# Performance work log

Hardware: AMD Instinct MI355X
Metric: run time of the kernel (lower is better)

## Reference

```python
import jax, jax.numpy as jnp
import numpy as np

B, S, E, NH = 2, 1024, 2048, 16
DH = E // NH
EPS = 1e-6

def setup_inputs() -> dict:
    key = jax.random.key(0)
    ks = jax.random.split(key, 6)
    q = jax.random.normal(ks[0], (B, S, E), dtype=jnp.float32)
    k = jax.random.normal(ks[1], (B, S, E), dtype=jnp.float32)
    v = jax.random.normal(ks[2], (B, S, E), dtype=jnp.float32)
    Wi = jax.random.normal(ks[3], (3 * E, NH), dtype=jnp.float32) * 0.02
    bi = jax.random.normal(ks[4], (NH,), dtype=jnp.float32) * 0.1
    Wf = jax.random.normal(ks[5], (3 * E, NH), dtype=jnp.float32) * 0.02
    bf = jnp.linspace(3.0, 6.0, NH, dtype=jnp.float32)  # bias_linspace_initializer(3,6)
    ln_scale = jnp.ones((E,), dtype=jnp.float32)
    return {"q": q, "k": k, "v": v, "Wi": Wi, "bi": bi, "Wf": Wf, "bf": bf, "ln_scale": ln_scale}

def _mlstm_forward(q, k, v, Wi, bi, Wf, bf, ln_scale):
    b, s, e = q.shape
    nh = Wi.shape[1]
    dh = e // nh
    x = jnp.concatenate([q, k, v], axis=-1)                     # (B,S,3E)
    ig = (x @ Wi + bi).transpose(0, 2, 1)[..., None]            # (B,NH,S,1)
    fg = (x @ Wf + bf).transpose(0, 2, 1)[..., None]            # (B,NH,S,1)
    split = lambda t: t.reshape(b, s, nh, dh).transpose(0, 2, 1, 3)
    qh, kh, vh = split(q), split(k), split(v)                   # (B,NH,S,DH)
    # parallel_stabilized_simple backend
    log_f = jax.nn.log_sigmoid(fg)                              # (B,NH,S,1)
    log_f_cum = jnp.concatenate(
        [jnp.zeros((b, nh, 1, 1), q.dtype), jnp.cumsum(log_f, axis=2)], axis=2
    )                                                           # (B,NH,S+1,1)
    # D[i,j] = cumsum[i] - cumsum[j] on causal part
    fg_mat = log_f_cum - jnp.transpose(log_f_cum, (0, 1, 3, 2)) # (B,NH,S+1,S+1)
    ltr = jnp.tril(jnp.ones((s, s), dtype=bool))
    log_fg = jnp.where(ltr, fg_mat[:, :, 1:, 1:], -jnp.inf)     # (B,NH,S,S)
    log_D = log_fg + jnp.transpose(ig, (0, 1, 3, 2))            # + i_j per column
    max_log_D = jnp.max(log_D, axis=-1, keepdims=True)          # (B,NH,S,1)
    D = jnp.exp(log_D - max_log_D)
    qk = jnp.einsum('bhsd,bhtd->bhst', qh, kh) / jnp.sqrt(jnp.asarray(dh, q.dtype))
    C = qk * D                                                  # (B,NH,S,S)
    normalizer = jnp.maximum(jnp.abs(C.sum(-1, keepdims=True)), jnp.exp(-max_log_D))
    Cn = C / (normalizer + EPS)
    h = jnp.einsum('bhst,bhtd->bhsd', Cn, vh)                   # (B,NH,S,DH)
    # MultiHeadLayerNorm: normalize over DH per head, scale (no bias)
    mu = h.mean(-1, keepdims=True)
    var = ((h - mu) ** 2).mean(-1, keepdims=True)
    hn = (h - mu) * jax.lax.rsqrt(var + EPS)
    hn = hn * ln_scale.reshape(1, nh, 1, dh)
    return hn.transpose(0, 2, 1, 3).reshape(b, s, e)            # (B,S,E)

def reference(q, k, v, Wi, bi, Wf, bf, ln_scale):
    return _mlstm_forward(q, k, v, Wi, bi, Wf, bf, ln_scale)
```

## Files before the change

### kernel.cpp

```cpp
#include <hip/hip_runtime.h>
#include <hip/hip_bf16.h>

#define B_   2
#define S_   1024
#define E_   2048
#define NH_  16
#define DH_  128
#define EPS_ 1e-6f

using half8   = __attribute__((ext_vector_type(8))) _Float16;
using floatx4 = __attribute__((ext_vector_type(4))) float;

__device__ __forceinline__ half8 cvt8h(const float* __restrict__ p) {
    float4 a = *(const float4*)p;
    float4 b = *(const float4*)(p + 4);
    half8 r;
    r[0] = (_Float16)a.x; r[1] = (_Float16)a.y;
    r[2] = (_Float16)a.z; r[3] = (_Float16)a.w;
    r[4] = (_Float16)b.x; r[5] = (_Float16)b.y;
    r[6] = (_Float16)b.z; r[7] = (_Float16)b.w;
    return r;
}

__global__ __launch_bounds__(256, 4) void gates_kernel(
    const float* __restrict__ q, const float* __restrict__ k,
    const float* __restrict__ v, const float* __restrict__ Wi,
    const float* __restrict__ Wf, float* __restrict__ pre_i,
    float* __restrict__ pre_f, _Float16* __restrict__ qhg,
    _Float16* __restrict__ khg, _Float16* __restrict__ vtg)
{
    __shared__ __attribute__((aligned(16))) _Float16 xs[32 * 264];
    __shared__ __attribute__((aligned(16))) _Float16 wt[32 * 264];

    const int t    = threadIdx.x;
    const int w    = t >> 6, lane = t & 63, quad = lane >> 4, l15 = lane & 15;
    const int mw   = w & 1, nw = w >> 1;
    const int m0   = blockIdx.x * 32;
    const int by   = blockIdx.y;
    const int kbase = by * 768;
    const int bblk = m0 >> 10;
    const int s0   = m0 & 1023;

    floatx4 acc = {0.f, 0.f, 0.f, 0.f};

    for (int c = 0; c < 3; ++c) {
        __syncthreads();
        const int e0   = kbase + c * 256;
        const int tsel = e0 >> 11;
        const int el0  = e0 & 2047;
        const float* xb = (tsel == 0) ? q : (tsel == 1) ? k : v;
        _Float16* fout = (tsel == 0) ? qhg : khg;
        #pragma unroll
        for (int i = 0; i < 4; ++i) {
            int g = t + i * 256;
            int row = g >> 5, grp = g & 31;
            half8 s8 = cvt8h(xb + (size_t)(m0 + row) * E_ + el0 + grp * 8);
            *(half8*)(&xs[row * 264 + grp * 8]) = s8;
            if (tsel < 2) {
                int el = el0 + grp * 8;
                int h  = el >> 7, d = el & 127;
                *(half8*)(fout + ((size_t)(bblk * NH_ + h) * S_ + s0 + row) * DH_ + d) = s8;
            }
        }
        {
            const int kk = t;
            const float* wiRow = Wi + (size_t)(e0 + kk) * NH_;
            const float* wfRow = Wf + (size_t)(e0 + kk) * NH_;
            float wif[16], wff[16];
            #pragma unroll
            for (int i4 = 0; i4 < 4; ++i4) {
                float4 a = *(const float4*)(wiRow + i4 * 4);
                wif[i4*4+0]=a.x; wif[i4*4+1]=a.y; wif[i4*4+2]=a.z; wif[i4*4+3]=a.w;
                float4 b = *(const float4*)(wfRow + i4 * 4);
                wff[i4*4+0]=b.x; wff[i4*4+1]=b.y; wff[i4*4+2]=b.z; wff[i4*4+3]=b.w;
            }
            #pragma unroll
            for (int hh = 0; hh < 16; ++hh) wt[hh * 264 + kk]        = (_Float16)wif[hh];
            #pragma unroll
            for (int hh = 0; hh < 16; ++hh) wt[(16 + hh) * 264 + kk] = (_Float16)wff[hh];
        }
        __syncthreads();
        if (tsel == 2) {
            const int col = t;
            const int el  = el0 + col;
            const int h   = el >> 7, d = el & 127;
            _Float16 tmp[32];
            #pragma unroll
            for (int r = 0; r < 32; ++r) tmp[r] = xs[r * 264 + col];
            const size_t vo = ((size_t)(bblk * NH_ + h) * DH_ + d) * S_ + s0;
            #pragma unroll
            for (int i = 0; i < 4; ++i)
                *(half8*)(vtg + vo + i * 8) = *(half8*)(&tmp[i * 8]);
        }
        #pragma unroll
        for (int ks = 0; ks < 8; ++ks) {
            half8 af = *(const half8*)(&xs[(mw * 16 + l15) * 264 + ks * 32 + quad * 8]);
            half8 bw = *(const half8*)(&wt[(nw * 16 + l15) * 264 + ks * 32 + quad * 8]);
            acc = __builtin_amdgcn_mfma_f32_16x16x32_f16(af, bw, acc, 0, 0, 0);
        }
    }
    #pragma unroll
    for (int reg = 0; reg < 4; ++reg) {
        int m   = m0 + mw * 16 + quad * 4 + reg;
        int b   = m >> 10, s = m & 1023;
        int col = nw * 16 + l15;
        float vacc = acc[reg];
        if (col < 16)
            pre_i[((size_t)(by * 32 + b * NH_ + col)) * S_ + s] = vacc;
        else
            pre_f[((size_t)(by * 32 + b * NH_ + col - 16)) * S_ + s] = vacc;
    }
}

__global__ __launch_bounds__(1024, 1) void scan_kernel(
    const float* __restrict__ pre_i, const float* __restrict__ pre_f,
    float* __restrict__ Aj, float* __restrict__ Cq,
    float* __restrict__ NFo, const float* __restrict__ bi,
    const float* __restrict__ bfb)
{
    __shared__ float wsumF[16], wmaxA[16];
    const int bh   = blockIdx.x;
    const int h    = bh & 15;
    const int t    = threadIdx.x;
    const int lane = t & 63, wv = t >> 6;

    float igv = bi[h], x = bfb[h];
    #pragma unroll
    for (int y = 0; y < 8; ++y) {
        igv += pre_i[((size_t)(y * 32 + bh)) * S_ + t];
        x   += pre_f[((size_t)(y * 32 + bh)) * S_ + t];
    }
    float lfv = (x >= 0.f) ? -log1pf(__expf(-x)) : (x - log1pf(__expf(x)));

    float sc = lfv;
    #pragma unroll
    for (int off = 1; off < 64; off <<= 1) {
        float o = __shfl_up(sc, off);
        if (lane >= off) sc += o;
    }
    if (lane == 63) wsumF[wv] = sc;
    __syncthreads();
    float Foff = 0.f;
    for (int i = 0; i < wv; ++i) Foff += wsumF[i];
    float F = Foff + sc;
    float a = igv - F;

    float ms = a;
    #pragma unroll
    for (int off = 1; off < 64; off <<= 1) {
        float o = __shfl_up(ms, off);
        if (lane >= off) ms = fmaxf(ms, o);
    }
    if (lane == 63) wmaxA[wv] = ms;
    __syncthreads();
    float Moff = -3.0e38f;
    for (int i = 0; i < wv; ++i) Moff = fmaxf(Moff, wmaxA[i]);
    float M = fmaxf(Moff, ms);

    size_t o = (size_t)bh * S_ + t;
    Aj[o]  = a;
    Cq[o]  = -M;
    NFo[o] = expf(fminf(-(F + M), 80.f));
}

__global__ __launch_bounds__(256, 1) void attn_kernel(
    const _Float16* __restrict__ qh, const _Float16* __restrict__ kh,
    const _Float16* __restrict__ vtg, const float* __restrict__ Aj,
    const float* __restrict__ Cq, const float* __restrict__ NFi,
    const float* __restrict__ lnsc, float* __restrict__ out)
{
    __shared__ __attribute__((aligned(16))) _Float16 Ks[64 * 136];
    __shared__ __attribute__((aligned(16))) _Float16 Vt[128 * 72];
    __shared__ __attribute__((aligned(16))) _Float16 Pb[128 * 72];
    __shared__ float aj[64];

    const int t    = threadIdx.x;
    const int w    = t >> 6, lane = t & 63, quad = lane >> 4, l15 = lane & 15;
    const int bid  = blockIdx.x;
    const int bh   = bid & 31;
    const int qpi  = bid >> 5;
    const int b    = bh >> 4, h = bh & 15;
    const int myq  = (w < 2) ? qpi : (15 - qpi);
    const int ktN  = 15 - qpi;
    const int qrow0 = myq * 64 + (w & 1) * 32;
    const int prow0 = w * 32;
    const int krow = t >> 2, kd0 = (t & 3) * 32;
    const int vd   = t >> 1, vj0 = (t & 1) * 32;

    float ci_r[2][4], nfv_r[2][4];
    #pragma unroll
    for (int s = 0; s < 2; ++s)
        #pragma unroll
        for (int reg = 0; reg < 4; ++reg) {
            int rl = qrow0 + s * 16 + quad * 4 + reg;
            ci_r[s][reg]  = Cq[(size_t)bh * S_ + rl];
            nfv_r[s][reg] = NFi[(size_t)bh * S_ + rl];
        }
    half8 aq[2][4];
    #pragma unroll
    for (int s = 0; s < 2; ++s) {
        const _Float16* qrow = qh + ((size_t)bh * S_ + qrow0 + s * 16 + l15) * DH_;
        #pragma unroll
        for (int ks = 0; ks < 4; ++ks)
            aq[s][ks] = *(const half8*)(qrow + ks * 32 + quad * 8);
    }

    half8 kreg[4], vreg[4];
    float ajreg = 0.f;
    {
        const _Float16* kp = kh + ((size_t)bh * S_ + krow) * DH_ + kd0;
        const _Float16* vp = vtg + ((size_t)bh * DH_ + vd) * S_ + vj0;
        #pragma unroll
        for (int i = 0; i < 4; ++i) { kreg[i] = *(const half8*)(kp + i * 8);
                                      vreg[i] = *(const half8*)(vp + i * 8); }
    }
    if (t < 64) ajreg = Aj[(size_t)bh * S_ + t];

    #pragma unroll
    for (int i = 0; i < 4; ++i) {
        *(half8*)(&Ks[krow * 136 + kd0 + i * 8]) = kreg[i];
        *(half8*)(&Vt[vd * 72 + vj0 + i * 8])    = vreg[i];
    }
    if (t < 64) aj[t] = ajreg;
    __syncthreads();

    floatx4 acc_h[2][8];
    #pragma unroll
    for (int s = 0; s < 2; ++s)
        #pragma unroll
        for (int i = 0; i < 8; ++i) acc_h[s][i] = (floatx4){0.f, 0.f, 0.f, 0.f};
    float lrun[2][4] = {{0.f, 0.f, 0.f, 0.f}, {0.f, 0.f, 0.f, 0.f}};
    const float rscale = 0.08838834764831845f;

    for (int kt = 0; kt <= ktN; ++kt) {
        if (kt < ktN) {
            const int j0n = (kt + 1) * 64;
            const _Float16* kp = kh + ((size_t)bh * S_ + j0n + krow) * DH_ + kd0;
            const _Float16* vp = vtg + ((size_t)bh * DH_ + vd) * S_ + j0n + vj0;
            #pragma unroll
            for (int i = 0; i < 4; ++i) { kreg[i] = *(const half8*)(kp + i * 8);
                                          vreg[i] = *(const half8*)(vp + i * 8); }
            if (t < 64) ajreg = Aj[(size_t)bh * S_ + j0n + t];
        }

        if (kt <= myq) {
            floatx4 sacc[2][4];
            #pragma unroll
            for (int s = 0; s < 2; ++s)
                #pragma unroll
                for (int nt = 0; nt < 4; ++nt) sacc[s][nt] = (floatx4){0.f, 0.f, 0.f, 0.f};
            #pragma unroll
            for (int ks = 0; ks < 4; ++ks) {
                #pragma unroll
                for (int nt = 0; nt < 4; ++nt) {
                    half8 bk = *(const half8*)(&Ks[(nt * 16 + l15) * 136 + ks * 32 + quad * 8]);
                    sacc[0][nt] = __builtin_amdgcn_mfma_f32_16x16x32_f16(aq[0][ks], bk, sacc[0][nt], 0, 0, 0);
                    sacc[1][nt] = __builtin_amdgcn_mfma_f32_16x16x32_f16(aq[1][ks], bk, sacc[1][nt], 0, 0, 0);
                }
            }
            const bool diag = (kt == myq);
            #pragma unroll
            for (int nt = 0; nt < 4; ++nt) {
                int jl = nt * 16 + l15;
                float a_j = aj[jl];
                #pragma unroll
                for (int s = 0; s < 2; ++s) {
                    #pragma unroll
                    for (int reg = 0; reg < 4; ++reg) {
                        int rloc = (w & 1) * 32 + s * 16 + quad * 4 + reg;
                        float p = 0.f;
                        if (!diag || (jl <= rloc))
                            p = sacc[s][nt][reg] * rscale * __expf(fminf(ci_r[s][reg] + a_j, 0.f));
                        lrun[s][reg] += p;
                        Pb[(prow0 + s * 16 + quad * 4 + reg) * 72 + jl] = (_Float16)p;
                    }
                }
            }
            #pragma unroll
            for (int ks2 = 0; ks2 < 2; ++ks2) {
                half8 ap0 = *(const half8*)(&Pb[(prow0 + l15) * 72 + ks2 * 32 + quad * 8]);
                half8 ap1 = *(const half8*)(&Pb[(prow0 + 16 + l15) * 72 + ks2 * 32 + quad * 8]);
                #pragma unroll
                for (int nt2 = 0; nt2 < 8; ++nt2) {
                    half8 bv = *(const half8*)(&Vt[(nt2 * 16 + l15) * 72 + ks2 * 32 + quad * 8]);
                    acc_h[0][nt2] = __builtin_amdgcn_mfma_f32_16x16x32_f16(ap0, bv, acc_h[0][nt2], 0, 0, 0);
                    acc_h[1][nt2] = __builtin_amdgcn_mfma_f32_16x16x32_f16(ap1, bv, acc_h[1][nt2], 0, 0, 0);
                }
            }
        }

        __syncthreads();
        if (kt < ktN) {
            #pragma unroll
            for (int i = 0; i < 4; ++i) {
                *(half8*)(&Ks[krow * 136 + kd0 + i * 8]) = kreg[i];
                *(half8*)(&Vt[vd * 72 + vj0 + i * 8])    = vreg[i];
            }
            if (t < 64) aj[t] = ajreg;
            __syncthreads();
        }
    }

    #pragma unroll
    for (int s = 0; s < 2; ++s) {
        #pragma unroll
        for (int reg = 0; reg < 4; ++reg) {
            float l = lrun[s][reg];
            #pragma unroll
            for (int off = 1; off < 16; off <<= 1) l += __shfl_xor(l, off);
            int rl = qrow0 + s * 16 + quad * 4 + reg;
            float nrm = fmaxf(fabsf(l), nfv_r[s][reg]) + EPS_;
            float inv = 1.f / nrm;
            float hv[8];
            float sum = 0.f, sq = 0.f;
            #pragma unroll
            for (int nt2 = 0; nt2 < 8; ++nt2) {
                float x = acc_h[s][nt2][reg] * inv;
                hv[nt2] = x; sum += x; sq += x * x;
            }
            #pragma unroll
            for (int off = 1; off < 16; off <<= 1) {
                sum += __shfl_xor(sum, off);
                sq  += __shfl_xor(sq, off);
            }
            float mean = sum * (1.f / 128.f);
            float var  = fmaxf(sq * (1.f / 128.f) - mean * mean, 0.f);
            float rstd = rsqrtf(var + EPS_);
            size_t orow = ((size_t)b * S_ + rl) * E_ + h * DH_;
            #pragma unroll
            for (int nt2 = 0; nt2 < 8; ++nt2) {
                int d = nt2 * 16 + l15;
                out[orow + d] = (hv[nt2] - mean) * rstd * lnsc[h * DH_ + d];
            }
        }
    }
}

extern "C" void kernel_launch(void* const* d_in, const int* in_sizes, int n_in,
                              void* d_out, int out_size, void* d_ws, size_t ws_size,
                              hipStream_t stream)
{
    const float* q    = (const float*)d_in[0];
    const float* k    = (const float*)d_in[1];
    const float* v    = (const float*)d_in[2];
    const float* Wi   = (const float*)d_in[3];
    const float* bi   = (const float*)d_in[4];
    const float* Wf   = (const float*)d_in[5];
    const float* bfb  = (const float*)d_in[6];
    const float* lnsc = (const float*)d_in[7];
    float* out        = (float*)d_out;

    const int NS  = B_ * NH_ * S_;
    float* pre_i = (float*)d_ws;
    float* pre_f = pre_i + 8 * NS;
    float* Aj    = pre_f + 8 * NS;
    float* Cq    = Aj + NS;
    float* NFa   = Cq + NS;
    _Float16* qh  = (_Float16*)(NFa + NS);
    _Float16* kh  = qh + (size_t)32 * S_ * DH_;
    _Float16* vtg = kh + (size_t)32 * S_ * DH_;

    gates_kernel<<<dim3(64, 8), 256, 0, stream>>>(q, k, v, Wi, Wf, pre_i, pre_f,
                                                  qh, kh, vtg);
    scan_kernel<<<dim3(32), 1024, 0, stream>>>(pre_i, pre_f, Aj, Cq, NFa, bi, bfb);
    attn_kernel<<<dim3(256), 256, 0, stream>>>(qh, kh, vtg, Aj, Cq, NFa, lnsc, out);
}
```

Baseline: 162.8 us.

## Split attention work across 2x2 warp grid with one query tile per block

```diff
diff --git a/kernel.cpp b/kernel.cpp
--- a/kernel.cpp
+++ b/kernel.cpp
@@ -163,7 +163,7 @@
     NFo[o] = expf(fminf(-(F + M), 80.f));
 }
 
-__global__ __launch_bounds__(256, 1) void attn_kernel(
+__global__ __launch_bounds__(256, 2) void attn_kernel(
     const _Float16* __restrict__ qh, const _Float16* __restrict__ kh,
     const _Float16* __restrict__ vtg, const float* __restrict__ Aj,
     const float* __restrict__ Cq, const float* __restrict__ NFi,
@@ -171,19 +171,21 @@
 {
     __shared__ __attribute__((aligned(16))) _Float16 Ks[64 * 136];
     __shared__ __attribute__((aligned(16))) _Float16 Vt[128 * 72];
-    __shared__ __attribute__((aligned(16))) _Float16 Pb[128 * 72];
+    __shared__ __attribute__((aligned(16))) _Float16 Pb[64 * 72];
     __shared__ float aj[64];
+    __shared__ float lpart[2][2][32];
+    __shared__ float spart[2][2][32];
+    __shared__ float qpart[2][2][32];
 
     const int t    = threadIdx.x;
     const int w    = t >> 6, lane = t & 63, quad = lane >> 4, l15 = lane & 15;
-    const int bid  = blockIdx.x;
-    const int bh   = bid & 31;
-    const int qpi  = bid >> 5;
+    const int mw   = w & 1, nw = w >> 1;
+    const int L    = blockIdx.x;
+    int qi, bh;
+    if (L < 256) { qi = L >> 5;                bh = L & 31; }
+    else         { qi = 15 - ((L - 256) >> 5); bh = (L - 256) & 31; }
     const int b    = bh >> 4, h = bh & 15;
-    const int myq  = (w < 2) ? qpi : (15 - qpi);
-    const int ktN  = 15 - qpi;
-    const int qrow0 = myq * 64 + (w & 1) * 32;
-    const int prow0 = w * 32;
+    const int q0   = qi * 64;
     const int krow = t >> 2, kd0 = (t & 3) * 32;
     const int vd   = t >> 1, vj0 = (t & 1) * 32;
 
@@ -192,14 +194,14 @@
     for (int s = 0; s < 2; ++s)
         #pragma unroll
         for (int reg = 0; reg < 4; ++reg) {
-            int rl = qrow0 + s * 16 + quad * 4 + reg;
+            int rl = q0 + mw * 32 + s * 16 + quad * 4 + reg;
             ci_r[s][reg]  = Cq[(size_t)bh * S_ + rl];
             nfv_r[s][reg] = NFi[(size_t)bh * S_ + rl];
         }
     half8 aq[2][4];
     #pragma unroll
     for (int s = 0; s < 2; ++s) {
-        const _Float16* qrow = qh + ((size_t)bh * S_ + qrow0 + s * 16 + l15) * DH_;
+        const _Float16* qrow = qh + ((size_t)bh * S_ + q0 + mw * 32 + s * 16 + l15) * DH_;
         #pragma unroll
         for (int ks = 0; ks < 4; ++ks)
             aq[s][ks] = *(const half8*)(qrow + ks * 32 + quad * 8);
@@ -224,16 +226,16 @@
     if (t < 64) aj[t] = ajreg;
     __syncthreads();
 
-    floatx4 acc_h[2][8];
-    #pragma unroll
-    for (int s = 0; s < 2; ++s)
-        #pragma unroll
-        for (int i = 0; i < 8; ++i) acc_h[s][i] = (floatx4){0.f, 0.f, 0.f, 0.f};
+    floatx4 acc_h[2][4];
+    #pragma unroll
+    for (int s = 0; s < 2; ++s)
+        #pragma unroll
+        for (int i = 0; i < 4; ++i) acc_h[s][i] = (floatx4){0.f, 0.f, 0.f, 0.f};
     float lrun[2][4] = {{0.f, 0.f, 0.f, 0.f}, {0.f, 0.f, 0.f, 0.f}};
     const float rscale = 0.08838834764831845f;
 
-    for (int kt = 0; kt <= ktN; ++kt) {
-        if (kt < ktN) {
+    for (int kt = 0; kt <= qi; ++kt) {
+        if (kt < qi) {
             const int j0n = (kt + 1) * 64;
             const _Float16* kp = kh + ((size_t)bh * S_ + j0n + krow) * DH_ + kd0;
             const _Float16* vp = vtg + ((size_t)bh * DH_ + vd) * S_ + j0n + vj0;
@@ -243,97 +245,129 @@
             if (t < 64) ajreg = Aj[(size_t)bh * S_ + j0n + t];
         }
 
-        if (kt <= myq) {
-            floatx4 sacc[2][4];
-            #pragma unroll
-            for (int s = 0; s < 2; ++s)
-                #pragma unroll
-                for (int nt = 0; nt < 4; ++nt) sacc[s][nt] = (floatx4){0.f, 0.f, 0.f, 0.f};
+        const bool diag = (kt == qi);
+        floatx4 sacc[2][2];
+        #pragma unroll
+        for (int s = 0; s < 2; ++s)
+            #pragma unroll
+            for (int n = 0; n < 2; ++n) sacc[s][n] = (floatx4){0.f, 0.f, 0.f, 0.f};
+        if (!(diag && mw == 0 && nw == 1)) {
+            __builtin_amdgcn_s_setprio(1);
             #pragma unroll
             for (int ks = 0; ks < 4; ++ks) {
                 #pragma unroll
-                for (int nt = 0; nt < 4; ++nt) {
-                    half8 bk = *(const half8*)(&Ks[(nt * 16 + l15) * 136 + ks * 32 + quad * 8]);
-                    sacc[0][nt] = __builtin_amdgcn_mfma_f32_16x16x32_f16(aq[0][ks], bk, sacc[0][nt], 0, 0, 0);
-                    sacc[1][nt] = __builtin_amdgcn_mfma_f32_16x16x32_f16(aq[1][ks], bk, sacc[1][nt], 0, 0, 0);
+                for (int n = 0; n < 2; ++n) {
+                    half8 bk = *(const half8*)(&Ks[(nw * 32 + n * 16 + l15) * 136 + ks * 32 + quad * 8]);
+                    sacc[0][n] = __builtin_amdgcn_mfma_f32_16x16x32_f16(aq[0][ks], bk, sacc[0][n], 0, 0, 0);
+                    sacc[1][n] = __builtin_amdgcn_mfma_f32_16x16x32_f16(aq[1][ks], bk, sacc[1][n], 0, 0, 0);
                 }
             }
-            const bool diag = (kt == myq);
-            #pragma unroll
-            for (int nt = 0; nt < 4; ++nt) {
-                int jl = nt * 16 + l15;
-                float a_j = aj[jl];
+            __builtin_amdgcn_s_setprio(0);
+        }
+        #pragma unroll
+        for (int n = 0; n < 2; ++n) {
+            int jl = nw * 32 + n * 16 + l15;
+            float a_j = aj[jl];
+            #pragma unroll
+            for (int s = 0; s < 2; ++s) {
                 #pragma unroll
-                for (int s = 0; s < 2; ++s) {
-                    #pragma unroll
-                    for (int reg = 0; reg < 4; ++reg) {
-                        int rloc = (w & 1) * 32 + s * 16 + quad * 4 + reg;
-                        float p = 0.f;
-                        if (!diag || (jl <= rloc))
-                            p = sacc[s][nt][reg] * rscale * __expf(fminf(ci_r[s][reg] + a_j, 0.f));
-                        lrun[s][reg] += p;
-                        Pb[(prow0 + s * 16 + quad * 4 + reg) * 72 + jl] = (_Float16)p;
-                    }
+                for (int reg = 0; reg < 4; ++reg) {
+                    int rloc = mw * 32 + s * 16 + quad * 4 + reg;
+                    float p = 0.f;
+                    if (!diag || (jl <= rloc))
+                        p = sacc[s][n][reg] * rscale * __expf(fminf(ci_r[s][reg] + a_j, 0.f));
+                    lrun[s][reg] += p;
+                    Pb[rloc * 72 + jl] = (_Float16)p;
                 }
             }
-            #pragma unroll
-            for (int ks2 = 0; ks2 < 2; ++ks2) {
-                half8 ap0 = *(const half8*)(&Pb[(prow0 + l15) * 72 + ks2 * 32 + quad * 8]);
-                half8 ap1 = *(const half8*)(&Pb[(prow0 + 16 + l15) * 72 + ks2 * 32 + quad * 8]);
-                #pragma unroll
-                for (int nt2 = 0; nt2 < 8; ++nt2) {
-                    half8 bv = *(const half8*)(&Vt[(nt2 * 16 + l15) * 72 + ks2 * 32 + quad * 8]);
-                    acc_h[0][nt2] = __builtin_amdgcn_mfma_f32_16x16x32_f16(ap0, bv, acc_h[0][nt2], 0, 0, 0);
-                    acc_h[1][nt2] = __builtin_amdgcn_mfma_f32_16x16x32_f16(ap1, bv, acc_h[1][nt2], 0, 0, 0);
-                }
-            }
-        }
-
+        }
         __syncthreads();
-        if (kt < ktN) {
-            #pragma unroll
-            for (int i = 0; i < 4; ++i) {
+
+        if (kt < qi) {
+            #pragma unroll
+            for (int i = 0; i < 4; ++i)
                 *(half8*)(&Ks[krow * 136 + kd0 + i * 8]) = kreg[i];
-                *(half8*)(&Vt[vd * 72 + vj0 + i * 8])    = vreg[i];
-            }
             if (t < 64) aj[t] = ajreg;
-            __syncthreads();
-        }
-    }
-
-    #pragma unroll
-    for (int s = 0; s < 2; ++s) {
+        }
+        __builtin_amdgcn_s_setprio(1);
+        #pragma unroll
+        for (int ks2 = 0; ks2 < 2; ++ks2) {
+            half8 ap0 = *(const half8*)(&Pb[(mw * 32 + l15) * 72 + ks2 * 32 + quad * 8]);
+            half8 ap1 = *(const half8*)(&Pb[(mw * 32 + 16 + l15) * 72 + ks2 * 32 + quad * 8]);
+            #pragma unroll
+            for (int n = 0; n < 4; ++n) {
+                half8 bv = *(const half8*)(&Vt[(nw * 64 + n * 16 + l15) * 72 + ks2 * 32 + quad * 8]);
+                acc_h[0][n] = __builtin_amdgcn_mfma_f32_16x16x32_f16(ap0, bv, acc_h[0][n], 0, 0, 0);
+                acc_h[1][n] = __builtin_amdgcn_mfma_f32_16x16x32_f16(ap1, bv, acc_h[1][n], 0, 0, 0);
+            }
+        }
+        __builtin_amdgcn_s_setprio(0);
+        __syncthreads();
+
+        if (kt < qi) {
+            #pragma unroll
+            for (int i = 0; i < 4; ++i)
+                *(half8*)(&Vt[vd * 72 + vj0 + i * 8]) = vreg[i];
+        }
+    }
+
+    #pragma unroll
+    for (int s = 0; s < 2; ++s)
         #pragma unroll
         for (int reg = 0; reg < 4; ++reg) {
             float l = lrun[s][reg];
-            #pragma unroll
-            for (int off = 1; off < 16; off <<= 1) l += __shfl_xor(l, off);
-            int rl = qrow0 + s * 16 + quad * 4 + reg;
-            float nrm = fmaxf(fabsf(l), nfv_r[s][reg]) + EPS_;
-            float inv = 1.f / nrm;
-            float hv[8];
+            l += __shfl_xor(l, 1); l += __shfl_xor(l, 2);
+            l += __shfl_xor(l, 4); l += __shfl_xor(l, 8);
+            if (l15 == 0) lpart[nw][mw][s * 16 + quad * 4 + reg] = l;
+        }
+    __syncthreads();
+    float inv_r[2][4];
+    #pragma unroll
+    for (int s = 0; s < 2; ++s)
+        #pragma unroll
+        for (int reg = 0; reg < 4; ++reg) {
+            int rr = s * 16 + quad * 4 + reg;
+            float ltot = lpart[0][mw][rr] + lpart[1][mw][rr];
+            inv_r[s][reg] = 1.f / (fmaxf(fabsf(ltot), nfv_r[s][reg]) + EPS_);
+        }
+    #pragma unroll
+    for (int s = 0; s < 2; ++s)
+        #pragma unroll
+        for (int reg = 0; reg < 4; ++reg) {
             float sum = 0.f, sq = 0.f;
             #pragma unroll
-            for (int nt2 = 0; nt2 < 8; ++nt2) {
-                float x = acc_h[s][nt2][reg] * inv;
-                hv[nt2] = x; sum += x; sq += x * x;
-            }
-            #pragma unroll
-            for (int off = 1; off < 16; off <<= 1) {
-                sum += __shfl_xor(sum, off);
-                sq  += __shfl_xor(sq, off);
-            }
+            for (int n = 0; n < 4; ++n) {
+                float x = acc_h[s][n][reg] * inv_r[s][reg];
+                sum += x; sq += x * x;
+            }
+            sum += __shfl_xor(sum, 1); sq += __shfl_xor(sq, 1);
+            sum += __shfl_xor(sum, 2); sq += __shfl_xor(sq, 2);
+            sum += __shfl_xor(sum, 4); sq += __shfl_xor(sq, 4);
+            sum += __shfl_xor(sum, 8); sq += __shfl_xor(sq, 8);
+            if (l15 == 0) {
+                spart[nw][mw][s * 16 + quad * 4 + reg] = sum;
+                qpart[nw][mw][s * 16 + quad * 4 + reg] = sq;
+            }
+        }
+    __syncthreads();
+    #pragma unroll
+    for (int s = 0; s < 2; ++s)
+        #pragma unroll
+        for (int reg = 0; reg < 4; ++reg) {
+            int rr   = s * 16 + quad * 4 + reg;
+            float sum = spart[0][mw][rr] + spart[1][mw][rr];
+            float sq  = qpart[0][mw][rr] + qpart[1][mw][rr];
             float mean = sum * (1.f / 128.f);
             float var  = fmaxf(sq * (1.f / 128.f) - mean * mean, 0.f);
             float rstd = rsqrtf(var + EPS_);
+            int rl = q0 + mw * 32 + rr;
             size_t orow = ((size_t)b * S_ + rl) * E_ + h * DH_;
             #pragma unroll
-            for (int nt2 = 0; nt2 < 8; ++nt2) {
-                int d = nt2 * 16 + l15;
-                out[orow + d] = (hv[nt2] - mean) * rstd * lnsc[h * DH_ + d];
-            }
-        }
-    }
+            for (int n = 0; n < 4; ++n) {
+                int d = nw * 64 + n * 16 + l15;
+                out[orow + d] = (acc_h[s][n][reg] * inv_r[s][reg] - mean) * rstd * lnsc[h * DH_ + d];
+            }
+        }
 }
 
 extern "C" void kernel_launch(void* const* d_in, const int* in_sizes, int n_in,
@@ -363,5 +397,5 @@
     gates_kernel<<<dim3(64, 8), 256, 0, stream>>>(q, k, v, Wi, Wf, pre_i, pre_f,
                                                   qh, kh, vtg);
     scan_kernel<<<dim3(32), 1024, 0, stream>>>(pre_i, pre_f, Aj, Cq, NFa, bi, bfb);
-    attn_kernel<<<dim3(256), 256, 0, stream>>>(qh, kh, vtg, Aj, Cq, NFa, lnsc, out);
+    attn_kernel<<<dim3(512), 256, 0, stream>>>(qh, kh, vtg, Aj, Cq, NFa, lnsc, out);
 }
```

New measurement: 145.6 us. 1.12x faster.
